# Optimization experiments

Measured on AMD Instinct MI355X. Metric: run time of the kernel, lower is better.

The kernel has to match this reference:

```python
import jax, jax.numpy as jnp
import numpy as np
from jax import lax

T, C_IN, H0, W0 = 15, 6, 160, 160
C1, C2 = 128, 256
K1, K2 = 5, 2
THR1, THR2 = 10.0, 1.0
KWTA, RAD = 8, 1
W_MEAN, W_STD = 0.8, 0.05


def setup_inputs() -> dict:
    key = jax.random.key(0)
    k1, k2, k3 = jax.random.split(key, 3)
    # cumulative binary spike wave: each input neuron fires at a random time (or never)
    t_fire = jax.random.randint(k1, (C_IN, H0, W0), 0, 2 * T)
    inp = (jnp.arange(T)[:, None, None, None] >= t_fire[None]).astype(jnp.float32)
    w1 = W_MEAN + W_STD * jax.random.normal(k2, (C1, C_IN, K1, K1), jnp.float32)
    w2 = W_MEAN + W_STD * jax.random.normal(k3, (C2, C1, K2, K2), jnp.float32)
    return {"inp": inp, "w1": w1, "w2": w2, "layer_idx": 2}


def _conv(x, w):
    # x: [T, C, H, W] (time acts as batch), VALID conv, no bias (SpykeTorch snn.Convolution)
    return lax.conv_general_dilated(x, w, (1, 1), 'VALID',
                                    dimension_numbers=('NCHW', 'OIHW', 'NCHW'))


def _pad(x, p):
    return jnp.pad(x, ((0, 0), (0, 0), (p, p), (p, p)))


def _pool(x):
    # sf.pooling(s, 2, 2, 1): max-pool kernel 2, stride 2, padding 1 per time step
    return lax.reduce_window(x, -jnp.inf, lax.max,
                             (1, 1, 2, 2), (1, 1, 2, 2),
                             ((0, 0), (0, 0), (1, 1), (1, 1)))


def _fire(v, thr):
    # sf.fire with return_thresholded_potentials=True: zero out sub-threshold potentials
    v = jnp.where(v < thr, 0.0, v)
    return jnp.sign(v), v


def _pointwise_inhibition(v):
    # v: [T, C, H, W] nonneg.  At each spatial position, the feature with the max
    t, c = v.shape[0], v.shape[1]
    max_vals = v.max(axis=1)                      # [T,H,W]
    max_idx = v.argmax(axis=1).astype(jnp.int32)  # [T,H,W] winner channel per time
    clamp = jnp.sign(max_vals)                    # [T,H,W] any-spike indicator
    earliest = jnp.clip(t - clamp.sum(axis=0).astype(jnp.int32), 0, t - 1)  # [H,W]
    winner = jnp.take_along_axis(max_idx, earliest[None], axis=0)[0]        # [H,W]
    alive = clamp[-1]                             # [H,W] 1 if any spike ever
    coef = (jnp.arange(c)[:, None, None] == winner[None]).astype(v.dtype) * alive
    return v * coef[None]


def _get_k_winners(v, s, kwta, rad):
    # Greedy k-WTA with per-feature and spatial (radius) inhibition (NMS-like).
    t, c, h, w = v.shape
    earliest = jnp.clip(t - s.sum(axis=0).astype(jnp.int32), 0, t - 1)  # [C,H,W]
    vals = jnp.take_along_axis(v, earliest[None], axis=0)[0]            # potential at first spike
    trunc = s * vals
    big = trunc.max() * t                                               # earlier-spike dominance term
    trunc = trunc + s * big
    total = trunc.sum(axis=0)                                           # [C,H,W]

    ch_ids = jnp.arange(c)
    row_ids = jnp.arange(h)
    col_ids = jnp.arange(w)

    def step(total, _):
        idx = jnp.argmax(total.reshape(-1))
        mv = total.reshape(-1)[idx]
        f = (idx // (h * w)).astype(jnp.int32)
        rem = idx % (h * w)
        r = (rem // w).astype(jnp.int32)
        col = (rem % w).astype(jnp.int32)
        active = mv != 0
        kill = ((ch_ids == f)[:, None, None]
                | ((jnp.abs(row_ids - r) <= rad)[:, None]
                   & (jnp.abs(col_ids - col) <= rad)[None, :])[None])
        new_total = jnp.where(active, jnp.where(kill, 0.0, total), total)
        winner = jnp.where(active, jnp.stack([f, r, col]), -1)
        return new_total, winner

    _, winners = lax.scan(step, total, None, length=kwta)
    return winners  # [kwta, 3] (feature,row,col), -1 rows = inactive


def reference(inp, w1, w2, layer_idx):
    # training path, layer_idx == 2 (deepest branch)
    x = _pad(inp, 2)                       # [T,6,164,164]
    v = _conv(x, w1)                       # [T,128,160,160]
    s, v = _fire(v, THR1)
    s_in = _pad(_pool(s), 1)               # [T,128,83,83]
    s_in = _pointwise_inhibition(s_in)
    v = _conv(s_in, w2)                    # [T,256,82,82]
    s, v = _fire(v, THR2)
    v = _pointwise_inhibition(v)
    s = jnp.sign(v)
    winners = _get_k_winners(v, s, KWTA, RAD)
    return s, v, winners
```

## Files before the change

kernel.cpp:

```cpp
#include <hip/hip_runtime.h>

#define T_ 15
#define CIN 6
#define H0 160
#define W0 160
#define C1_ 128
#define C2_ 256
#define HP 83
#define H2 82
#define NPIX (H0*W0)
#define NIN (CIN*NPIX)
#define NPOS (H2*H2)
#define NS (T_*C2_*NPOS)
#define THR1 10.0f
#define THR2 1.0f
#define NF1 1024
#define NF2 3072

__global__ __launch_bounds__(256) void k_mega(const float* __restrict__ inp,
                                              const float* __restrict__ w1,
                                              const float* __restrict__ w2,
                                              unsigned int* __restrict__ maskg,
                                              float* __restrict__ w1T,
                                              float* __restrict__ w2T,
                                              unsigned int* __restrict__ bigbits,
                                              uint4* __restrict__ fill_dst,
                                              size_t nA, int nf) {
    __shared__ unsigned char tft[CIN * 20 * 20];
    __shared__ int cnt[16 * 256];
    int b = blockIdx.x;
    int tid = threadIdx.x;

    if (b < 100) {
        int ty0 = (b / 10) * 16, tx0 = (b % 10) * 16;
        for (int i = tid; i < CIN * 400; i += 256) {
            int ci = i / 400, rem = i % 400;
            int ly = rem / 20, lx = rem % 20;
            int y = ty0 + ly - 2, x = tx0 + lx - 2;
            unsigned char tv = 15;
            if ((unsigned)y < (unsigned)H0 && (unsigned)x < (unsigned)W0) {
                float c = 0.f;
                int base = ci * NPIX + y * W0 + x;
#pragma unroll
                for (int t = 0; t < T_; t++) c += inp[(size_t)t * NIN + base];
                tv = (unsigned char)(15 - (int)(c + 0.5f));
            }
            tft[i] = tv;
        }
        __syncthreads();

        int tyl = tid >> 4, txl = tid & 15;
        int pix = (ty0 + tyl) * W0 + (tx0 + txl);
        int* col = cnt + tid;

#pragma unroll
        for (int w = 0; w < 5; w++) {
            int j0 = w * 32, j1 = (w == 4) ? 150 : (j0 + 32);
#pragma unroll
            for (int q = 0; q < 16; q++) col[q * 256] = 0;
#pragma unroll 32
            for (int j = j0; j < j1; j++) {
                int ci = j / 25, r = j % 25, ky = r / 5, kx = r % 5;
                int tfv = tft[ci * 400 + (tyl + ky) * 20 + (txl + kx)];
                col[tfv * 256] |= 1u << (j & 31);
            }
#pragma unroll
            for (int t = 0; t < 15; t++)
                maskg[(size_t)(t * 5 + w) * NPIX + pix] = (unsigned)col[t * 256];
        }
    } else if (b < 175) {
        if (b == 100 && tid == 0) *bigbits = 0u;
        int idx = (b - 100) * 256 + tid;
        int j = idx >> 7, c = idx & 127;
        w1T[idx] = w1[c * 150 + j];
    } else if (b < 687) {
        int idx = (b - 175) * 256 + tid;
        int o = idx & 255, kcc = idx >> 8;
        int cc = kcc & 127, k = kcc >> 7;
        w2T[idx] = w2[o * 512 + cc * 4 + k];
    } else {
        size_t stride = (size_t)nf * 256;
        uint4 z = make_uint4(0u, 0u, 0u, 0u);
        for (size_t i = (size_t)(b - 687) * 256 + tid; i < nA; i += stride)
            fill_dst[i] = z;
    }
}

__global__ __launch_bounds__(256) void k1_main(const unsigned int* __restrict__ maskg,
                                               const float* __restrict__ w1T,
                                               unsigned char* __restrict__ fst1,
                                               uint4* __restrict__ fill_dst,
                                               size_t nA, size_t n16, int nf) {
    int b = blockIdx.x;
    int tid = threadIdx.x;
    if (b >= 6400) {
        size_t stride = (size_t)nf * 256;
        uint4 z = make_uint4(0u, 0u, 0u, 0u);
        for (size_t i = nA + (size_t)(b - 6400) * 256 + tid; i < n16; i += stride)
            fill_dst[i] = z;
        return;
    }
    int pix = b * 4 + (tid >> 6);
    int lane = tid & 63;
    const float* wb = w1T + 2 * lane;

    float v0 = 0.f, v1 = 0.f;
    int f0 = 15, f1 = 15;
    for (int t = 0; t < 15; ++t) {
        float b0 = 0.f, b1 = 0.f;
#pragma unroll
        for (int w = 0; w < 5; ++w) {
            unsigned int m = maskg[(size_t)(t * 5 + w) * NPIX + pix];
            int base = w * 32;
            while (m) {
                int j = base + __builtin_ctz(m);
                m &= m - 1;
                float2 ww = *(const float2*)(wb + j * C1_);
                b0 += ww.x; b1 += ww.y;
            }
        }
        v0 += b0; v1 += b1;
        f0 = (f0 == 15 && v0 >= THR1) ? t : f0;
        f1 = (f1 == 15 && v1 >= THR1) ? t : f1;
        if (__all((f0 < 15) & (f1 < 15))) break;
    }
    *(uchar2*)(fst1 + (size_t)pix * C1_ + 2 * lane) =
        make_uchar2((unsigned char)f0, (unsigned char)f1);
}

__global__ __launch_bounds__(256) void k2_pool(const unsigned char* __restrict__ fst1,
                                               unsigned char* __restrict__ win_t,
                                               unsigned char* __restrict__ win_ch) {
    int pos = blockIdx.x * 4 + (threadIdx.x >> 6);
    int lane = threadIdx.x & 63;
    if (pos >= HP * HP) return;
    int py = pos / HP, px = pos % HP;
    if (py == 0 || py == HP - 1 || px == 0 || px == HP - 1) {
        if (lane == 0) { win_t[pos] = 15; win_ch[pos] = 0; }
        return;
    }
    int y0 = 2 * py - 3, x0 = 2 * px - 3;
    int m0 = 15, m1 = 15;
#pragma unroll
    for (int dy = 0; dy < 2; dy++) {
        int y = y0 + dy;
        if ((unsigned)y < (unsigned)H0) {
#pragma unroll
            for (int dx = 0; dx < 2; dx++) {
                int x = x0 + dx;
                if ((unsigned)x < (unsigned)W0) {
                    uchar2 f = *(const uchar2*)(fst1 + (size_t)(y * W0 + x) * C1_ + 2 * lane);
                    m0 = f.x < m0 ? f.x : m0;
                    m1 = f.y < m1 ? f.y : m1;
                }
            }
        }
    }
    int k0 = (m0 << 8) | (2 * lane);
    int k1 = (m1 << 8) | (2 * lane + 1);
    int key = k0 < k1 ? k0 : k1;
#pragma unroll
    for (int off = 32; off > 0; off >>= 1) {
        int other = __shfl_xor(key, off);
        key = other < key ? other : key;
    }
    if (lane == 0) {
        win_t[pos] = (unsigned char)(key >> 8);
        win_ch[pos] = (unsigned char)(key & 255);
    }
}

__global__ __launch_bounds__(256) void kz_fill(uint4* __restrict__ dst, size_t n16,
                                               unsigned int* __restrict__ bigbits) {
    size_t stride = (size_t)gridDim.x * 256;
    uint4 z = make_uint4(0u, 0u, 0u, 0u);
    for (size_t i = (size_t)blockIdx.x * 256 + threadIdx.x; i < n16; i += stride)
        dst[i] = z;
    if (blockIdx.x == 0 && threadIdx.x == 0) *bigbits = 0u;
}

__global__ __launch_bounds__(256) void k3_conv2(const unsigned char* __restrict__ win_t,
                                                const unsigned char* __restrict__ win_ch,
                                                const float* __restrict__ w2T,
                                                float* __restrict__ s_out,
                                                float* __restrict__ v_out,
                                                float* __restrict__ vals,
                                                int* __restrict__ nsp_arr,
                                                int* __restrict__ ow_arr,
                                                unsigned int* __restrict__ bigbits) {
    int p = blockIdx.x * 4 + (threadIdx.x >> 6);
    int lane = threadIdx.x & 63;
    int y2 = p / H2, x2 = p % H2;

    int tj[4]; int ccv[4];
#pragma unroll
    for (int k = 0; k < 4; k++) {
        int dy = k >> 1, dx = k & 1;
        int pi = (y2 + dy) * HP + (x2 + dx);
        tj[k] = win_t[pi];
        ccv[k] = win_ch[pi];
    }

    float wq[4][4];
    unsigned int mq[4];
    unsigned int lane_or = 0u;
#pragma unroll
    for (int q = 0; q < 4; q++) {
        int ch = q * 64 + lane;
#pragma unroll
        for (int k = 0; k < 4; k++)
            wq[q][k] = (tj[k] < 15) ? w2T[(k * C1_ + ccv[k]) * 256 + ch] : 0.0f;
        unsigned int m = 0u;
#pragma unroll
        for (int t = 0; t < T_; t++) {
            float v = 0.f;
#pragma unroll
            for (int k = 0; k < 4; k++) v += (t >= tj[k]) ? wq[q][k] : 0.f;
            m |= (v >= THR2) ? (1u << t) : 0u;
        }
        mq[q] = m;
        lane_or |= m;
    }

#pragma unroll
    for (int off = 32; off > 0; off >>= 1) lane_or |= __shfl_xor(lane_or, off);
    unsigned int om = lane_or;
    int count = __popc(om & 0x7FFFu);
    int earliest = 15 - count;
    earliest = earliest < 0 ? 0 : (earliest > 14 ? 14 : earliest);
    int alive = (om >> 14) & 1;

    unsigned long long best = 0ull;
    float bw0 = 0.f, bw1 = 0.f, bw2 = 0.f, bw3 = 0.f;
    unsigned int bm = 0u;
#pragma unroll
    for (int q = 0; q < 4; q++) {
        int ch = q * 64 + lane;
        float v = 0.f;
#pragma unroll
        for (int k = 0; k < 4; k++) v += (earliest >= tj[k]) ? wq[q][k] : 0.f;
        float zval = (v < THR2) ? 0.f : v;
        unsigned long long key =
            ((unsigned long long)__float_as_uint(zval) << 16) |
            (unsigned long long)(1023 - ch);
        if (key > best) {
            best = key;
            bw0 = wq[q][0]; bw1 = wq[q][1]; bw2 = wq[q][2]; bw3 = wq[q][3];
            bm = mq[q];
        }
    }
    unsigned long long gbest = best;
#pragma unroll
    for (int off = 32; off > 0; off >>= 1) {
        unsigned long long other = __shfl_xor(gbest, off);
        gbest = other > gbest ? other : gbest;
    }

    if (alive) {
        int wo = 1023 - (int)(gbest & 0xFFFFull);
        if ((wo & 63) == lane && best == gbest) {
            int nsp = __popc(bm & 0x7FFFu);
            int e2 = 15 - nsp;
            e2 = e2 < 0 ? 0 : (e2 > 14 ? 14 : e2);
            float vv = 0.f;
#pragma unroll
            for (int k = 0; k < 4; k++) {
                float wk = (k == 0) ? bw0 : (k == 1) ? bw1 : (k == 2) ? bw2 : bw3;
                vv += (e2 >= tj[k]) ? wk : 0.f;
            }
            vv = (vv < THR2) ? 0.f : vv;
            vals[p] = vv; nsp_arr[p] = nsp; ow_arr[p] = wo;
            if (nsp > 0) atomicMax(bigbits, __float_as_uint(vv));
#pragma unroll
            for (int t = 0; t < T_; t++) {
                if ((bm >> t) & 1u) {
                    float vt = 0.f;
                    vt += (t >= tj[0]) ? bw0 : 0.f;
                    vt += (t >= tj[1]) ? bw1 : 0.f;
                    vt += (t >= tj[2]) ? bw2 : 0.f;
                    vt += (t >= tj[3]) ? bw3 : 0.f;
                    int idx = ((t * C2_ + wo) * H2 + y2) * H2 + x2;
                    v_out[idx] = vt;
                    s_out[idx] = 1.0f;
                }
            }
        }
    } else if (lane == 0) {
        vals[p] = 0.f; nsp_arr[p] = 0; ow_arr[p] = 0;
    }
}

__global__ __launch_bounds__(1024) void k4_kwta(const float* __restrict__ vals,
                                                const int* __restrict__ nsp,
                                                const int* __restrict__ ow,
                                                const unsigned int* __restrict__ bigbits,
                                                float* __restrict__ wout) {
    __shared__ float tot[NPOS];
    __shared__ short och[NPOS];
    __shared__ unsigned long long amax;
    int tid = threadIdx.x;
    float big = __uint_as_float(*bigbits) * 15.0f;

    for (int p = tid; p < NPOS; p += 1024) {
        int n = nsp[p];
        tot[p] = (n > 0) ? (float)n * (vals[p] + big) : 0.0f;
        och[p] = (short)ow[p];
    }
    if (tid == 0) amax = 0ull;
    __syncthreads();

    for (int it = 0; it < 8; it++) {
        unsigned long long best = 0ull;
        for (int p = tid; p < NPOS; p += 1024) {
            float tv = tot[p];
            if (tv > 0.0f) {
                unsigned int k = (unsigned)och[p] * (unsigned)NPOS + (unsigned)p;
                unsigned long long pk =
                    ((unsigned long long)__float_as_uint(tv) << 21) |
                    (unsigned long long)(0x1FFFFFu - k);
                best = pk > best ? pk : best;
            }
        }
#pragma unroll
        for (int off = 32; off > 0; off >>= 1) {
            unsigned long long other = __shfl_xor(best, off);
            best = other > best ? other : best;
        }
        if ((tid & 63) == 0) atomicMax(&amax, best);
        __syncthreads();
        unsigned long long mx = amax;
        __syncthreads();
        if (tid == 0) amax = 0ull;

        if (mx == 0ull) {
            if (tid == 0) {
                wout[it * 3 + 0] = -1.f; wout[it * 3 + 1] = -1.f; wout[it * 3 + 2] = -1.f;
            }
        } else {
            unsigned int k = 0x1FFFFFu - (unsigned)(mx & 0x1FFFFFull);
            int f = (int)(k / NPOS), pp = (int)(k % NPOS);
            int r = pp / H2, col = pp % H2;
            if (tid == 0) {
                wout[it * 3 + 0] = (float)f; wout[it * 3 + 1] = (float)r; wout[it * 3 + 2] = (float)col;
            }
            for (int p = tid; p < NPOS; p += 1024) {
                int pr = p / H2, pc = p % H2;
                bool kill = (och[p] == (short)f) ||
                            (pr >= r - 1 && pr <= r + 1 && pc >= col - 1 && pc <= col + 1);
                if (kill) tot[p] = 0.0f;
            }
        }
        __syncthreads();
    }
}

extern "C" void kernel_launch(void* const* d_in, const int* in_sizes, int n_in,
                              void* d_out, int out_size, void* d_ws, size_t ws_size,
                              hipStream_t stream) {
    const float* inp = (const float*)d_in[0];
    const float* w1  = (const float*)d_in[1];
    const float* w2  = (const float*)d_in[2];

    float* out = (float*)d_out;
    float* s_out = out;
    float* v_out = out + (size_t)NS;
    float* wnr   = out + 2 * (size_t)NS;

    size_t need = (size_t)15 << 20;
    bool big_ws = ws_size >= need;
    char* scratch = big_ws ? (char*)d_ws
                           : (char*)d_out + (size_t)NS * sizeof(float);
    unsigned int* maskg = (unsigned int*)scratch;
    unsigned char* fst1 = (unsigned char*)(scratch + (8 << 20));
    float* w1T = (float*)(scratch + (12 << 20));
    float* w2T = (float*)(scratch + (13 << 20));
    char* smol = big_ws ? (char*)d_ws + (14 << 20) : (char*)d_ws;
    unsigned char* win_t  = (unsigned char*)smol;
    unsigned char* win_ch = (unsigned char*)smol + 8192;
    float* vals = (float*)(smol + 16384);
    int*   nsp  = (int*)(smol + 49152);
    int*   ow   = (int*)(smol + 81920);
    unsigned int* bigbits = (unsigned int*)(smol + 114688);

    size_t n16 = (size_t)out_size / 4;
    size_t nA  = big_ws ? n16 / 4 : 0;
    int nf1 = big_ws ? NF1 : 0;
    int nf2 = big_ws ? NF2 : 0;

    hipLaunchKernelGGL(k_mega, dim3(687 + nf1), dim3(256), 0, stream,
                       inp, w1, w2, maskg, w1T, w2T, bigbits, (uint4*)d_out, nA, nf1);
    hipLaunchKernelGGL(k1_main, dim3(6400 + nf2), dim3(256), 0, stream,
                       maskg, w1T, fst1, (uint4*)d_out, nA, n16, nf2);
    hipLaunchKernelGGL(k2_pool, dim3((HP * HP + 3) / 4), dim3(256), 0, stream,
                       fst1, win_t, win_ch);
    if (!big_ws)
        hipLaunchKernelGGL(kz_fill, dim3(4096), dim3(256), 0, stream,
                           (uint4*)d_out, n16, bigbits);
    hipLaunchKernelGGL(k3_conv2, dim3(NPOS / 4), dim3(256), 0, stream,
                       win_t, win_ch, w2T, s_out, v_out, vals, nsp, ow, bigbits);
    hipLaunchKernelGGL(k4_kwta, dim3(1), dim3(1024), 0, stream, vals, nsp, ow, bigbits, wnr);
}
```

Baseline: 199.5 us.

## Fold output zero-fill into k1_main compute blocks instead of extra fill blocks

```diff
diff --git a/kernel.cpp b/kernel.cpp
--- a/kernel.cpp
+++ b/kernel.cpp
@@ -14,8 +14,6 @@
 #define NS (T_*C2_*NPOS)
 #define THR1 10.0f
 #define THR2 1.0f
-#define NF1 1024
-#define NF2 3072
 
 __global__ __launch_bounds__(256) void k_mega(const float* __restrict__ inp,
                                               const float* __restrict__ w1,
@@ -23,9 +21,7 @@
                                               unsigned int* __restrict__ maskg,
                                               float* __restrict__ w1T,
                                               float* __restrict__ w2T,
-                                              unsigned int* __restrict__ bigbits,
-                                              uint4* __restrict__ fill_dst,
-                                              size_t nA, int nf) {
+                                              unsigned int* __restrict__ bigbits) {
     __shared__ unsigned char tft[CIN * 20 * 20];
     __shared__ int cnt[16 * 256];
     int b = blockIdx.x;
@@ -73,16 +69,11 @@
         int idx = (b - 100) * 256 + tid;
         int j = idx >> 7, c = idx & 127;
         w1T[idx] = w1[c * 150 + j];
-    } else if (b < 687) {
+    } else {
         int idx = (b - 175) * 256 + tid;
         int o = idx & 255, kcc = idx >> 8;
         int cc = kcc & 127, k = kcc >> 7;
         w2T[idx] = w2[o * 512 + cc * 4 + k];
-    } else {
-        size_t stride = (size_t)nf * 256;
-        uint4 z = make_uint4(0u, 0u, 0u, 0u);
-        for (size_t i = (size_t)(b - 687) * 256 + tid; i < nA; i += stride)
-            fill_dst[i] = z;
     }
 }
 
@@ -90,16 +81,19 @@
                                                const float* __restrict__ w1T,
                                                unsigned char* __restrict__ fst1,
                                                uint4* __restrict__ fill_dst,
-                                               size_t nA, size_t n16, int nf) {
+                                               size_t n16) {
     int b = blockIdx.x;
     int tid = threadIdx.x;
-    if (b >= 6400) {
-        size_t stride = (size_t)nf * 256;
+
+    if (n16) {
+        size_t per = (n16 + 6399) / 6400;
+        size_t i = (size_t)b * per + tid;
+        size_t e = (size_t)(b + 1) * per;
+        if (e > n16) e = n16;
         uint4 z = make_uint4(0u, 0u, 0u, 0u);
-        for (size_t i = nA + (size_t)(b - 6400) * 256 + tid; i < n16; i += stride)
-            fill_dst[i] = z;
-        return;
-    }
+        for (; i < e; i += 256) fill_dst[i] = z;
+    }
+
     int pix = b * 4 + (tid >> 6);
     int lane = tid & 63;
     const float* wb = w1T + 2 * lane;
@@ -383,14 +377,12 @@
     unsigned int* bigbits = (unsigned int*)(smol + 114688);
 
     size_t n16 = (size_t)out_size / 4;
-    size_t nA  = big_ws ? n16 / 4 : 0;
-    int nf1 = big_ws ? NF1 : 0;
-    int nf2 = big_ws ? NF2 : 0;
-
-    hipLaunchKernelGGL(k_mega, dim3(687 + nf1), dim3(256), 0, stream,
-                       inp, w1, w2, maskg, w1T, w2T, bigbits, (uint4*)d_out, nA, nf1);
-    hipLaunchKernelGGL(k1_main, dim3(6400 + nf2), dim3(256), 0, stream,
-                       maskg, w1T, fst1, (uint4*)d_out, nA, n16, nf2);
+    size_t n16_k1 = big_ws ? n16 : 0;
+
+    hipLaunchKernelGGL(k_mega, dim3(687), dim3(256), 0, stream,
+                       inp, w1, w2, maskg, w1T, w2T, bigbits);
+    hipLaunchKernelGGL(k1_main, dim3(6400), dim3(256), 0, stream,
+                       maskg, w1T, fst1, (uint4*)d_out, n16_k1);
     hipLaunchKernelGGL(k2_pool, dim3((HP * HP + 3) / 4), dim3(256), 0, stream,
                        fst1, win_t, win_ch);
     if (!big_ws)
```

Result: faster. 195.5 us, median of 2 (-2.0%).
